# Optimization experiments

Measured on AMD Instinct MI355X. Metric: run time of the kernel, lower is better.

The kernel has to match this reference:

```python
import jax, jax.numpy as jnp
import numpy as np

N_NODES = 100000
N_EDGES = 300000
NUM_GRAPHS = 2000
IN_DIM = 82
HIDDEN = 256


def _gcn_conv(x, src, dst, dinv, W, b):
    # GCNConv: out = D^-1/2 (A + I) D^-1/2 (x W) + b
    xW = x @ W  # [N, H]
    norm = dinv[src] * dinv[dst]  # [E]
    agg = jax.ops.segment_sum(xW[src] * norm[:, None], dst, num_segments=N_NODES)
    self_loop = xW * (dinv * dinv)[:, None]
    return agg + self_loop + b


def setup_inputs() -> dict:
    key = jax.random.key(0)
    ks = jax.random.split(key, 8)
    x = jax.random.normal(ks[0], (N_NODES, IN_DIM), dtype=jnp.float32)
    edge_index = jax.random.randint(ks[1], (2, N_EDGES), 0, N_NODES, dtype=jnp.int64)
    batch = jnp.sort(jax.random.randint(ks[2], (N_NODES,), 0, NUM_GRAPHS, dtype=jnp.int64))
    W1 = jax.random.normal(ks[3], (IN_DIM, HIDDEN), dtype=jnp.float32) * (1.0 / np.sqrt(IN_DIM))
    W2 = jax.random.normal(ks[4], (HIDDEN, HIDDEN), dtype=jnp.float32) * (1.0 / np.sqrt(HIDDEN))
    W3 = jax.random.normal(ks[5], (HIDDEN, HIDDEN), dtype=jnp.float32) * (1.0 / np.sqrt(HIDDEN))
    b1 = jnp.zeros((HIDDEN,), jnp.float32)
    b2 = jnp.zeros((HIDDEN,), jnp.float32)
    b3 = jnp.zeros((HIDDEN,), jnp.float32)
    return {"x": x, "edge_index": edge_index, "batch": batch, "num_graphs": NUM_GRAPHS,
            "W1": W1, "b1": b1, "W2": W2, "b2": b2, "W3": W3, "b3": b3}


def reference(x, edge_index, batch, num_graphs, W1, b1, W2, b2, W3, b3):
    src, dst = edge_index[0], edge_index[1]
    # symmetric normalization with added self-loops (PyG gcn_norm)
    deg = jax.ops.segment_sum(jnp.ones_like(dst, dtype=x.dtype), dst, num_segments=N_NODES) + 1.0
    dinv = jax.lax.rsqrt(deg)
    h = jax.nn.relu(_gcn_conv(x, src, dst, dinv, W1, b1))
    h = jax.nn.relu(_gcn_conv(h, src, dst, dinv, W2, b2))
    h = jax.nn.relu(_gcn_conv(h, src, dst, dinv, W3, b3))
    return jax.ops.segment_max(h, batch, num_segments=num_graphs)  # [G, H]
```

## Files before the change

kernel.cpp:

```cpp
#include <hip/hip_runtime.h>
#include <cstdint>
#include <cstddef>

#define N_NODES 100000
#define N_EDGES 300000
#define N_GRAPHS 2000
#define HID 256
#define INDIM 82
#define K1PAD 128
#define N_TILES ((N_NODES + 255) / 256)
#define SCAN_CHUNK 2048
#define NBLK_SCAN ((N_NODES + SCAN_CHUNK - 1) / SCAN_CHUNK)

typedef __bf16 bf16x8 __attribute__((ext_vector_type(8)));
typedef float f32x4 __attribute__((ext_vector_type(4)));

__device__ __forceinline__ unsigned short f2bf(float f) {
    unsigned int u = __float_as_uint(f);
    u = (u + 0x7fffu + ((u >> 16) & 1u)) >> 16;
    return (unsigned short)u;
}
__device__ __forceinline__ float bf2f(unsigned short s) {
    return __uint_as_float(((unsigned int)s) << 16);
}

__global__ void k_cnt_init(int* cnt) {
    int i = blockIdx.x * 256 + threadIdx.x;
    if (i < N_NODES) cnt[i] = 0;
}

__global__ void k_cnt_acc(const int* __restrict__ ei, int* cnt) {
    int e = blockIdx.x * 256 + threadIdx.x;
    if (e < N_EDGES) atomicAdd(&cnt[ei[N_EDGES + e]], 1);
}

__global__ __launch_bounds__(256) void k_scan1(const int* __restrict__ cnt, int* __restrict__ off,
                                               int* __restrict__ partial) {
    __shared__ int sdata[256];
    const int base = blockIdx.x * SCAN_CHUNK;
    const int t = threadIdx.x;
    int v[8];
    int s = 0;
#pragma unroll
    for (int i = 0; i < 8; ++i) {
        int idx = base + t * 8 + i;
        v[i] = (idx < N_NODES) ? cnt[idx] : 0;
        s += v[i];
    }
    sdata[t] = s;
    __syncthreads();
    for (int d = 1; d < 256; d <<= 1) {
        int x = (t >= d) ? sdata[t - d] : 0;
        __syncthreads();
        sdata[t] += x;
        __syncthreads();
    }
    int run = sdata[t] - s;
#pragma unroll
    for (int i = 0; i < 8; ++i) {
        int idx = base + t * 8 + i;
        if (idx < N_NODES) off[idx] = run;
        run += v[i];
    }
    if (t == 255) partial[blockIdx.x] = sdata[255];
}

__global__ void k_scan2(int* partial) {
    if (threadIdx.x == 0 && blockIdx.x == 0) {
        int run = 0;
        for (int i = 0; i < NBLK_SCAN; ++i) {
            int v = partial[i];
            partial[i] = run;
            run += v;
        }
    }
}

__global__ void k_scan3(int* __restrict__ off, const int* __restrict__ partial,
                        int* __restrict__ cur, const int* __restrict__ cnt,
                        float* __restrict__ dinv) {
    int i = blockIdx.x * 256 + threadIdx.x;
    if (i < N_NODES) {
        int o = off[i] + partial[i >> 11];
        off[i] = o;
        cur[i] = o;
        dinv[i] = rsqrtf((float)cnt[i] + 1.0f);
    }
}

__global__ void k_fill(const int* __restrict__ ei, int* cur, int* __restrict__ csr_src) {
    int e = blockIdx.x * 256 + threadIdx.x;
    if (e < N_EDGES) {
        int s = ei[e];
        int d = ei[N_EDGES + e];
        int pos = atomicAdd(&cur[d], 1);
        csr_src[pos] = s;
    }
}

__global__ void k_bounds(const int* __restrict__ batch, int* __restrict__ gstart) {
    int g = blockIdx.x * 256 + threadIdx.x;
    if (g > N_GRAPHS) return;
    int lo = 0, hi = N_NODES;
    while (lo < hi) {
        int mid = (lo + hi) >> 1;
        if (batch[mid] < g) lo = mid + 1;
        else hi = mid;
    }
    gstart[g] = lo;
}

__global__ void k_xconv(const float* __restrict__ x, unsigned short* __restrict__ xb) {
    int i = blockIdx.x * 256 + threadIdx.x;
    if (i >= N_NODES * K1PAD) return;
    int node = i >> 7;
    int k = i & 127;
    xb[i] = (k < INDIM) ? f2bf(x[(size_t)node * INDIM + k]) : (unsigned short)0;
}

__global__ void k_wconv(const float* __restrict__ W, unsigned short* __restrict__ Wb,
                        int KPAD, int KSRC) {
    int i = blockIdx.x * 256 + threadIdx.x;
    if (i >= 256 * KPAD) return;
    int kc = i >> 13;
    int r = i & 8191;
    int nt = r >> 9;
    int r2 = r & 511;
    int lg = r2 >> 7;
    int lr = (r2 >> 3) & 15;
    int j = r2 & 7;
    int k = kc * 32 + lg * 8 + j;
    int n = nt * 16 + lr;
    Wb[i] = (k < KSRC) ? f2bf(W[(size_t)k * HID + n]) : (unsigned short)0;
}

template <int K>
__global__ __launch_bounds__(512) void k_gemm_mfma(const unsigned short* __restrict__ A,
                                                   const unsigned short* __restrict__ Wb,
                                                   const float* __restrict__ bias,
                                                   unsigned short* __restrict__ Cb) {
    constexpr int NK = K / 32;
    __shared__ __align__(16) unsigned short Wsh[K * HID];

    const int tid = threadIdx.x;
    const int w = tid >> 6;
    const int l = tid & 63;
    const int lr = l & 15;
    const int lg = l >> 4;

#pragma unroll
    for (int i = 0; i < K / 16; ++i) {
        int o = (i * 512 + tid) * 8;
        *reinterpret_cast<uint4*>(&Wsh[o]) = *reinterpret_cast<const uint4*>(Wb + o);
    }
    __syncthreads();

    float bv[16];
#pragma unroll
    for (int nt = 0; nt < 16; ++nt) bv[nt] = bias[nt * 16 + lr];

    for (int t = blockIdx.x; t < N_TILES; t += 256) {
        const int rowbase = t * 256 + w * 32;
        int r0 = rowbase + lr;
        int r1 = rowbase + 16 + lr;
        int r0c = r0 < N_NODES ? r0 : (N_NODES - 1);
        int r1c = r1 < N_NODES ? r1 : (N_NODES - 1);
        const unsigned short* a0p = A + (size_t)r0c * K + lg * 8;
        const unsigned short* a1p = A + (size_t)r1c * K + lg * 8;

        bf16x8 a0[NK], a1[NK];
#pragma unroll
        for (int kc = 0; kc < NK; ++kc) {
            a0[kc] = *reinterpret_cast<const bf16x8*>(a0p + kc * 32);
            a1[kc] = *reinterpret_cast<const bf16x8*>(a1p + kc * 32);
        }

        f32x4 acc0[16] = {};
        f32x4 acc1[16] = {};

#pragma unroll
        for (int kc = 0; kc < NK; ++kc) {
            const unsigned short* bfp = Wsh + kc * 8192 + l * 8;
#pragma unroll
            for (int nt = 0; nt < 16; ++nt) {
                bf16x8 bb = *reinterpret_cast<const bf16x8*>(bfp + nt * 512);
                acc0[nt] = __builtin_amdgcn_mfma_f32_16x16x32_bf16(a0[kc], bb, acc0[nt], 0, 0, 0);
                acc1[nt] = __builtin_amdgcn_mfma_f32_16x16x32_bf16(a1[kc], bb, acc1[nt], 0, 0, 0);
            }
        }

        int gr0 = rowbase + lg * 4;
#pragma unroll
        for (int j = 0; j < 4; ++j) {
            int gr = gr0 + j;
            if (gr < N_NODES) {
                size_t base = (size_t)gr * HID + lr;
#pragma unroll
                for (int nt = 0; nt < 16; ++nt)
                    Cb[base + nt * 16] = f2bf(fmaxf(acc0[nt][j] + bv[nt], 0.0f));
            }
            int gr2 = gr + 16;
            if (gr2 < N_NODES) {
                size_t base = (size_t)gr2 * HID + lr;
#pragma unroll
                for (int nt = 0; nt < 16; ++nt)
                    Cb[base + nt * 16] = f2bf(fmaxf(acc1[nt][j] + bv[nt], 0.0f));
            }
        }
    }
}

__global__ void k_aggregate256(const unsigned short* __restrict__ tb,
                               const float* __restrict__ dinv, const int* __restrict__ off,
                               const int* __restrict__ cnt, const int* __restrict__ csr_src,
                               unsigned short* __restrict__ ob) {
    int node = blockIdx.x * 4 + (threadIdx.x >> 6);
    if (node >= N_NODES) return;
    int lane = threadIdx.x & 63;
    float di = dinv[node];
    float s2 = di * di;
    ushort4 sv = *reinterpret_cast<const ushort4*>(&tb[(size_t)node * HID + lane * 4]);
    float4 acc = {bf2f(sv.x) * s2, bf2f(sv.y) * s2, bf2f(sv.z) * s2, bf2f(sv.w) * s2};

    int o0 = off[node];
    int n = cnt[node];
    int j = 0;
    for (; j + 1 < n; j += 2) {
        int s0 = csr_src[o0 + j];
        int s1 = csr_src[o0 + j + 1];
        float n0 = dinv[s0] * di;
        float n1 = dinv[s1] * di;
        ushort4 u0 = *reinterpret_cast<const ushort4*>(&tb[(size_t)s0 * HID + lane * 4]);
        ushort4 u1 = *reinterpret_cast<const ushort4*>(&tb[(size_t)s1 * HID + lane * 4]);
        acc.x = fmaf(n0, bf2f(u0.x), acc.x);
        acc.y = fmaf(n0, bf2f(u0.y), acc.y);
        acc.z = fmaf(n0, bf2f(u0.z), acc.z);
        acc.w = fmaf(n0, bf2f(u0.w), acc.w);
        acc.x = fmaf(n1, bf2f(u1.x), acc.x);
        acc.y = fmaf(n1, bf2f(u1.y), acc.y);
        acc.z = fmaf(n1, bf2f(u1.z), acc.z);
        acc.w = fmaf(n1, bf2f(u1.w), acc.w);
    }
    if (j < n) {
        int s0 = csr_src[o0 + j];
        float n0 = dinv[s0] * di;
        ushort4 u0 = *reinterpret_cast<const ushort4*>(&tb[(size_t)s0 * HID + lane * 4]);
        acc.x = fmaf(n0, bf2f(u0.x), acc.x);
        acc.y = fmaf(n0, bf2f(u0.y), acc.y);
        acc.z = fmaf(n0, bf2f(u0.z), acc.z);
        acc.w = fmaf(n0, bf2f(u0.w), acc.w);
    }
    ushort4 o;
    o.x = f2bf(acc.x);
    o.y = f2bf(acc.y);
    o.z = f2bf(acc.z);
    o.w = f2bf(acc.w);
    *reinterpret_cast<ushort4*>(&ob[(size_t)node * HID + lane * 4]) = o;
}

__global__ void k_aggregate128(const unsigned short* __restrict__ tb,
                               const float* __restrict__ dinv, const int* __restrict__ off,
                               const int* __restrict__ cnt, const int* __restrict__ csr_src,
                               unsigned short* __restrict__ ob) {
    int node = blockIdx.x * 4 + (threadIdx.x >> 6);
    if (node >= N_NODES) return;
    int lane = threadIdx.x & 63;
    float di = dinv[node];
    float s2 = di * di;
    ushort2 sv = *reinterpret_cast<const ushort2*>(&tb[(size_t)node * K1PAD + lane * 2]);
    float2 acc = {bf2f(sv.x) * s2, bf2f(sv.y) * s2};

    int o0 = off[node];
    int n = cnt[node];
    int j = 0;
    for (; j + 1 < n; j += 2) {
        int s0 = csr_src[o0 + j];
        int s1 = csr_src[o0 + j + 1];
        float n0 = dinv[s0] * di;
        float n1 = dinv[s1] * di;
        ushort2 u0 = *reinterpret_cast<const ushort2*>(&tb[(size_t)s0 * K1PAD + lane * 2]);
        ushort2 u1 = *reinterpret_cast<const ushort2*>(&tb[(size_t)s1 * K1PAD + lane * 2]);
        acc.x = fmaf(n0, bf2f(u0.x), acc.x);
        acc.y = fmaf(n0, bf2f(u0.y), acc.y);
        acc.x = fmaf(n1, bf2f(u1.x), acc.x);
        acc.y = fmaf(n1, bf2f(u1.y), acc.y);
    }
    if (j < n) {
        int s0 = csr_src[o0 + j];
        float n0 = dinv[s0] * di;
        ushort2 u0 = *reinterpret_cast<const ushort2*>(&tb[(size_t)s0 * K1PAD + lane * 2]);
        acc.x = fmaf(n0, bf2f(u0.x), acc.x);
        acc.y = fmaf(n0, bf2f(u0.y), acc.y);
    }
    ushort2 o;
    o.x = f2bf(acc.x);
    o.y = f2bf(acc.y);
    *reinterpret_cast<ushort2*>(&ob[(size_t)node * K1PAD + lane * 2]) = o;
}

__global__ void k_pool2(const unsigned short* __restrict__ hb, const int* __restrict__ gstart,
                        float* __restrict__ out) {
    int g = blockIdx.x;
    int lane = threadIdx.x;
    int s = gstart[g], e = gstart[g + 1];
    float4 m = {0.0f, 0.0f, 0.0f, 0.0f};
    for (int i = s; i < e; ++i) {
        ushort4 u = *reinterpret_cast<const ushort4*>(&hb[(size_t)i * HID + lane * 4]);
        m.x = fmaxf(m.x, bf2f(u.x));
        m.y = fmaxf(m.y, bf2f(u.y));
        m.z = fmaxf(m.z, bf2f(u.z));
        m.w = fmaxf(m.w, bf2f(u.w));
    }
    *reinterpret_cast<float4*>(&out[(size_t)g * HID + lane * 4]) = m;
}

extern "C" void kernel_launch(void* const* d_in, const int* in_sizes, int n_in,
                              void* d_out, int out_size, void* d_ws, size_t ws_size,
                              hipStream_t stream) {
    const float* x = (const float*)d_in[0];
    const int* ei = (const int*)d_in[1];
    const int* batch = (const int*)d_in[2];
    const float* W1 = (const float*)d_in[4];
    const float* b1 = (const float*)d_in[5];
    const float* W2 = (const float*)d_in[6];
    const float* b2 = (const float*)d_in[7];
    const float* W3 = (const float*)d_in[8];
    const float* b3 = (const float*)d_in[9];
    float* out = (float*)d_out;

    char* ws = (char*)d_ws;
    float* dinv = (float*)(ws);
    int* cnt = (int*)(ws + (512 << 10));
    int* off = (int*)(ws + (1024 << 10));
    int* cur = (int*)(ws + (1536 << 10));
    int* part = (int*)(ws + (2048 << 10));
    int* gstart = (int*)(ws + (2048 << 10) + 4096);
    int* csr_src = (int*)(ws + (2176 << 10));
    unsigned short* Wb1 = (unsigned short*)(ws + (3584 << 10));
    unsigned short* Wb2 = (unsigned short*)(ws + (3712 << 10));
    unsigned short* Wb3 = (unsigned short*)(ws + (3904 << 10));
    unsigned short* x_b = (unsigned short*)(ws + (4096 << 10));
    unsigned short* ag1_b = (unsigned short*)(ws + (4096 << 10) + 25600000);
    unsigned short* bufA = (unsigned short*)(ws + (4096 << 10) + 51200000);
    unsigned short* bufB = (unsigned short*)(ws + (4096 << 10) + 102400000);

    const int nblk_nodes = (N_NODES + 255) / 256;
    const int nblk_edges = (N_EDGES + 255) / 256;
    const int nblk_rows4 = (N_NODES + 3) / 4;

    k_cnt_init<<<nblk_nodes, 256, 0, stream>>>(cnt);
    k_cnt_acc<<<nblk_edges, 256, 0, stream>>>(ei, cnt);
    k_scan1<<<NBLK_SCAN, 256, 0, stream>>>(cnt, off, part);
    k_scan2<<<1, 64, 0, stream>>>(part);
    k_scan3<<<nblk_nodes, 256, 0, stream>>>(off, part, cur, cnt, dinv);
    k_fill<<<nblk_edges, 256, 0, stream>>>(ei, cur, csr_src);
    k_bounds<<<(N_GRAPHS + 256) / 256, 256, 0, stream>>>(batch, gstart);

    k_xconv<<<(N_NODES * K1PAD + 255) / 256, 256, 0, stream>>>(x, x_b);
    k_wconv<<<(256 * K1PAD + 255) / 256, 256, 0, stream>>>(W1, Wb1, K1PAD, INDIM);
    k_wconv<<<(256 * HID + 255) / 256, 256, 0, stream>>>(W2, Wb2, HID, HID);
    k_wconv<<<(256 * HID + 255) / 256, 256, 0, stream>>>(W3, Wb3, HID, HID);

    k_aggregate128<<<nblk_rows4, 256, 0, stream>>>(x_b, dinv, off, cnt, csr_src, ag1_b);
    k_gemm_mfma<K1PAD><<<256, 512, 0, stream>>>(ag1_b, Wb1, b1, bufA);

    k_aggregate256<<<nblk_rows4, 256, 0, stream>>>(bufA, dinv, off, cnt, csr_src, bufB);
    k_gemm_mfma<HID><<<256, 512, 0, stream>>>(bufB, Wb2, b2, bufA);

    k_aggregate256<<<nblk_rows4, 256, 0, stream>>>(bufA, dinv, off, cnt, csr_src, bufB);
    k_gemm_mfma<HID><<<256, 512, 0, stream>>>(bufB, Wb3, b3, bufA);

    k_pool2<<<N_GRAPHS, 64, 0, stream>>>(bufA, gstart, out);
}
```

Baseline: 282.7 us.

## Precompute edge norms in CSR, aggregate layer 1 from raw fp32 input, unroll gathers

The CSR fill kernel now stores a per-edge normalization weight, so the aggregation kernels no longer do a dependent dinv[src] gather per edge. The separate fp32-to-bf16 conversion of x is removed: the first-layer aggregation reads the 82-wide fp32 rows directly with 41 active lanes and writes padded bf16. The 256-wide aggregation loop is unrolled by four to keep more gathers in flight, and pooling uses 128 threads per graph. The cost is an extra 1.2 MB norm array and wider fp32 gathers in layer one.

```diff
diff --git a/kernel.cpp b/kernel.cpp
--- a/kernel.cpp
+++ b/kernel.cpp
@@ -88,13 +88,15 @@
     }
 }
 
-__global__ void k_fill(const int* __restrict__ ei, int* cur, int* __restrict__ csr_src) {
+__global__ void k_fill(const int* __restrict__ ei, const float* __restrict__ dinv, int* cur,
+                       int* __restrict__ csr_src, float* __restrict__ csr_norm) {
     int e = blockIdx.x * 256 + threadIdx.x;
     if (e < N_EDGES) {
         int s = ei[e];
         int d = ei[N_EDGES + e];
         int pos = atomicAdd(&cur[d], 1);
         csr_src[pos] = s;
+        csr_norm[pos] = dinv[s] * dinv[d];
     }
 }
 
@@ -108,14 +110,6 @@
         else hi = mid;
     }
     gstart[g] = lo;
-}
-
-__global__ void k_xconv(const float* __restrict__ x, unsigned short* __restrict__ xb) {
-    int i = blockIdx.x * 256 + threadIdx.x;
-    if (i >= N_NODES * K1PAD) return;
-    int node = i >> 7;
-    int k = i & 127;
-    xb[i] = (k < INDIM) ? f2bf(x[(size_t)node * INDIM + k]) : (unsigned short)0;
 }
 
 __global__ void k_wconv(const float* __restrict__ W, unsigned short* __restrict__ Wb,
@@ -213,105 +207,128 @@
 __global__ void k_aggregate256(const unsigned short* __restrict__ tb,
                                const float* __restrict__ dinv, const int* __restrict__ off,
                                const int* __restrict__ cnt, const int* __restrict__ csr_src,
+                               const float* __restrict__ csr_norm,
                                unsigned short* __restrict__ ob) {
     int node = blockIdx.x * 4 + (threadIdx.x >> 6);
     if (node >= N_NODES) return;
     int lane = threadIdx.x & 63;
+    const size_t lo = (size_t)lane * 4;
+    int o0 = off[node];
+    int n = cnt[node];
     float di = dinv[node];
     float s2 = di * di;
-    ushort4 sv = *reinterpret_cast<const ushort4*>(&tb[(size_t)node * HID + lane * 4]);
+    ushort4 sv = *reinterpret_cast<const ushort4*>(&tb[(size_t)node * HID + lo]);
     float4 acc = {bf2f(sv.x) * s2, bf2f(sv.y) * s2, bf2f(sv.z) * s2, bf2f(sv.w) * s2};
 
-    int o0 = off[node];
-    int n = cnt[node];
     int j = 0;
-    for (; j + 1 < n; j += 2) {
+    for (; j + 3 < n; j += 4) {
         int s0 = csr_src[o0 + j];
         int s1 = csr_src[o0 + j + 1];
-        float n0 = dinv[s0] * di;
-        float n1 = dinv[s1] * di;
-        ushort4 u0 = *reinterpret_cast<const ushort4*>(&tb[(size_t)s0 * HID + lane * 4]);
-        ushort4 u1 = *reinterpret_cast<const ushort4*>(&tb[(size_t)s1 * HID + lane * 4]);
-        acc.x = fmaf(n0, bf2f(u0.x), acc.x);
-        acc.y = fmaf(n0, bf2f(u0.y), acc.y);
-        acc.z = fmaf(n0, bf2f(u0.z), acc.z);
-        acc.w = fmaf(n0, bf2f(u0.w), acc.w);
-        acc.x = fmaf(n1, bf2f(u1.x), acc.x);
-        acc.y = fmaf(n1, bf2f(u1.y), acc.y);
-        acc.z = fmaf(n1, bf2f(u1.z), acc.z);
-        acc.w = fmaf(n1, bf2f(u1.w), acc.w);
-    }
-    if (j < n) {
+        int s2i = csr_src[o0 + j + 2];
+        int s3 = csr_src[o0 + j + 3];
+        float n0 = csr_norm[o0 + j];
+        float n1 = csr_norm[o0 + j + 1];
+        float n2 = csr_norm[o0 + j + 2];
+        float n3 = csr_norm[o0 + j + 3];
+        ushort4 u0 = *reinterpret_cast<const ushort4*>(&tb[(size_t)s0 * HID + lo]);
+        ushort4 u1 = *reinterpret_cast<const ushort4*>(&tb[(size_t)s1 * HID + lo]);
+        ushort4 u2 = *reinterpret_cast<const ushort4*>(&tb[(size_t)s2i * HID + lo]);
+        ushort4 u3 = *reinterpret_cast<const ushort4*>(&tb[(size_t)s3 * HID + lo]);
+        acc.x = fmaf(n0, bf2f(u0.x), acc.x); acc.y = fmaf(n0, bf2f(u0.y), acc.y);
+        acc.z = fmaf(n0, bf2f(u0.z), acc.z); acc.w = fmaf(n0, bf2f(u0.w), acc.w);
+        acc.x = fmaf(n1, bf2f(u1.x), acc.x); acc.y = fmaf(n1, bf2f(u1.y), acc.y);
+        acc.z = fmaf(n1, bf2f(u1.z), acc.z); acc.w = fmaf(n1, bf2f(u1.w), acc.w);
+        acc.x = fmaf(n2, bf2f(u2.x), acc.x); acc.y = fmaf(n2, bf2f(u2.y), acc.y);
+        acc.z = fmaf(n2, bf2f(u2.z), acc.z); acc.w = fmaf(n2, bf2f(u2.w), acc.w);
+        acc.x = fmaf(n3, bf2f(u3.x), acc.x); acc.y = fmaf(n3, bf2f(u3.y), acc.y);
+        acc.z = fmaf(n3, bf2f(u3.z), acc.z); acc.w = fmaf(n3, bf2f(u3.w), acc.w);
+    }
+    int rem = n - j;
+    if (rem & 2) {
         int s0 = csr_src[o0 + j];
-        float n0 = dinv[s0] * di;
-        ushort4 u0 = *reinterpret_cast<const ushort4*>(&tb[(size_t)s0 * HID + lane * 4]);
-        acc.x = fmaf(n0, bf2f(u0.x), acc.x);
-        acc.y = fmaf(n0, bf2f(u0.y), acc.y);
-        acc.z = fmaf(n0, bf2f(u0.z), acc.z);
-        acc.w = fmaf(n0, bf2f(u0.w), acc.w);
+        int s1 = csr_src[o0 + j + 1];
+        float n0 = csr_norm[o0 + j];
+        float n1 = csr_norm[o0 + j + 1];
+        ushort4 u0 = *reinterpret_cast<const ushort4*>(&tb[(size_t)s0 * HID + lo]);
+        ushort4 u1 = *reinterpret_cast<const ushort4*>(&tb[(size_t)s1 * HID + lo]);
+        acc.x = fmaf(n0, bf2f(u0.x), acc.x); acc.y = fmaf(n0, bf2f(u0.y), acc.y);
+        acc.z = fmaf(n0, bf2f(u0.z), acc.z); acc.w = fmaf(n0, bf2f(u0.w), acc.w);
+        acc.x = fmaf(n1, bf2f(u1.x), acc.x); acc.y = fmaf(n1, bf2f(u1.y), acc.y);
+        acc.z = fmaf(n1, bf2f(u1.z), acc.z); acc.w = fmaf(n1, bf2f(u1.w), acc.w);
+        j += 2;
+    }
+    if (rem & 1) {
+        int s0 = csr_src[o0 + j];
+        float n0 = csr_norm[o0 + j];
+        ushort4 u0 = *reinterpret_cast<const ushort4*>(&tb[(size_t)s0 * HID + lo]);
+        acc.x = fmaf(n0, bf2f(u0.x), acc.x); acc.y = fmaf(n0, bf2f(u0.y), acc.y);
+        acc.z = fmaf(n0, bf2f(u0.z), acc.z); acc.w = fmaf(n0, bf2f(u0.w), acc.w);
     }
     ushort4 o;
     o.x = f2bf(acc.x);
     o.y = f2bf(acc.y);
     o.z = f2bf(acc.z);
     o.w = f2bf(acc.w);
-    *reinterpret_cast<ushort4*>(&ob[(size_t)node * HID + lane * 4]) = o;
-}
-
-__global__ void k_aggregate128(const unsigned short* __restrict__ tb,
-                               const float* __restrict__ dinv, const int* __restrict__ off,
-                               const int* __restrict__ cnt, const int* __restrict__ csr_src,
-                               unsigned short* __restrict__ ob) {
+    *reinterpret_cast<ushort4*>(&ob[(size_t)node * HID + lo]) = o;
+}
+
+__global__ void k_aggxf(const float* __restrict__ x,
+                        const float* __restrict__ dinv, const int* __restrict__ off,
+                        const int* __restrict__ cnt, const int* __restrict__ csr_src,
+                        const float* __restrict__ csr_norm,
+                        unsigned short* __restrict__ ob) {
     int node = blockIdx.x * 4 + (threadIdx.x >> 6);
     if (node >= N_NODES) return;
     int lane = threadIdx.x & 63;
+    const bool act = lane < 41;
+    const size_t co = (size_t)lane * 2;
+    int o0 = off[node];
+    int n = cnt[node];
     float di = dinv[node];
     float s2 = di * di;
-    ushort2 sv = *reinterpret_cast<const ushort2*>(&tb[(size_t)node * K1PAD + lane * 2]);
-    float2 acc = {bf2f(sv.x) * s2, bf2f(sv.y) * s2};
-
-    int o0 = off[node];
-    int n = cnt[node];
-    int j = 0;
-    for (; j + 1 < n; j += 2) {
-        int s0 = csr_src[o0 + j];
-        int s1 = csr_src[o0 + j + 1];
-        float n0 = dinv[s0] * di;
-        float n1 = dinv[s1] * di;
-        ushort2 u0 = *reinterpret_cast<const ushort2*>(&tb[(size_t)s0 * K1PAD + lane * 2]);
-        ushort2 u1 = *reinterpret_cast<const ushort2*>(&tb[(size_t)s1 * K1PAD + lane * 2]);
-        acc.x = fmaf(n0, bf2f(u0.x), acc.x);
-        acc.y = fmaf(n0, bf2f(u0.y), acc.y);
-        acc.x = fmaf(n1, bf2f(u1.x), acc.x);
-        acc.y = fmaf(n1, bf2f(u1.y), acc.y);
-    }
-    if (j < n) {
-        int s0 = csr_src[o0 + j];
-        float n0 = dinv[s0] * di;
-        ushort2 u0 = *reinterpret_cast<const ushort2*>(&tb[(size_t)s0 * K1PAD + lane * 2]);
-        acc.x = fmaf(n0, bf2f(u0.x), acc.x);
-        acc.y = fmaf(n0, bf2f(u0.y), acc.y);
+    float2 acc = {0.0f, 0.0f};
+    if (act) {
+        float2 sv = *reinterpret_cast<const float2*>(&x[(size_t)node * INDIM + co]);
+        acc.x = sv.x * s2;
+        acc.y = sv.y * s2;
+        int j = 0;
+        for (; j + 1 < n; j += 2) {
+            int s0 = csr_src[o0 + j];
+            int s1 = csr_src[o0 + j + 1];
+            float n0 = csr_norm[o0 + j];
+            float n1 = csr_norm[o0 + j + 1];
+            float2 u0 = *reinterpret_cast<const float2*>(&x[(size_t)s0 * INDIM + co]);
+            float2 u1 = *reinterpret_cast<const float2*>(&x[(size_t)s1 * INDIM + co]);
+            acc.x = fmaf(n0, u0.x, acc.x); acc.y = fmaf(n0, u0.y, acc.y);
+            acc.x = fmaf(n1, u1.x, acc.x); acc.y = fmaf(n1, u1.y, acc.y);
+        }
+        if (j < n) {
+            int s0 = csr_src[o0 + j];
+            float n0 = csr_norm[o0 + j];
+            float2 u0 = *reinterpret_cast<const float2*>(&x[(size_t)s0 * INDIM + co]);
+            acc.x = fmaf(n0, u0.x, acc.x); acc.y = fmaf(n0, u0.y, acc.y);
+        }
     }
     ushort2 o;
     o.x = f2bf(acc.x);
     o.y = f2bf(acc.y);
-    *reinterpret_cast<ushort2*>(&ob[(size_t)node * K1PAD + lane * 2]) = o;
+    *reinterpret_cast<ushort2*>(&ob[(size_t)node * K1PAD + co]) = o;
 }
 
 __global__ void k_pool2(const unsigned short* __restrict__ hb, const int* __restrict__ gstart,
                         float* __restrict__ out) {
     int g = blockIdx.x;
-    int lane = threadIdx.x;
+    int w = threadIdx.x >> 6;
+    int lane = threadIdx.x & 63;
+    int col = w * 128 + lane * 2;
     int s = gstart[g], e = gstart[g + 1];
-    float4 m = {0.0f, 0.0f, 0.0f, 0.0f};
+    float2 m = {0.0f, 0.0f};
     for (int i = s; i < e; ++i) {
-        ushort4 u = *reinterpret_cast<const ushort4*>(&hb[(size_t)i * HID + lane * 4]);
+        ushort2 u = *reinterpret_cast<const ushort2*>(&hb[(size_t)i * HID + col]);
         m.x = fmaxf(m.x, bf2f(u.x));
         m.y = fmaxf(m.y, bf2f(u.y));
-        m.z = fmaxf(m.z, bf2f(u.z));
-        m.w = fmaxf(m.w, bf2f(u.w));
-    }
-    *reinterpret_cast<float4*>(&out[(size_t)g * HID + lane * 4]) = m;
+    }
+    *reinterpret_cast<float2*>(&out[(size_t)g * HID + col]) = m;
 }
 
 extern "C" void kernel_launch(void* const* d_in, const int* in_sizes, int n_in,
@@ -336,13 +353,13 @@
     int* part = (int*)(ws + (2048 << 10));
     int* gstart = (int*)(ws + (2048 << 10) + 4096);
     int* csr_src = (int*)(ws + (2176 << 10));
-    unsigned short* Wb1 = (unsigned short*)(ws + (3584 << 10));
-    unsigned short* Wb2 = (unsigned short*)(ws + (3712 << 10));
-    unsigned short* Wb3 = (unsigned short*)(ws + (3904 << 10));
-    unsigned short* x_b = (unsigned short*)(ws + (4096 << 10));
-    unsigned short* ag1_b = (unsigned short*)(ws + (4096 << 10) + 25600000);
-    unsigned short* bufA = (unsigned short*)(ws + (4096 << 10) + 51200000);
-    unsigned short* bufB = (unsigned short*)(ws + (4096 << 10) + 102400000);
+    float* csr_norm = (float*)(ws + (3392 << 10));
+    unsigned short* Wb1 = (unsigned short*)(ws + (4608 << 10));
+    unsigned short* Wb2 = (unsigned short*)(ws + (4736 << 10));
+    unsigned short* Wb3 = (unsigned short*)(ws + (4928 << 10));
+    unsigned short* ag1_b = (unsigned short*)(ws + (5120 << 10));
+    unsigned short* bufA = (unsigned short*)(ws + (5120 << 10) + 25600000);
+    unsigned short* bufB = (unsigned short*)(ws + (5120 << 10) + 76800000);
 
     const int nblk_nodes = (N_NODES + 255) / 256;
     const int nblk_edges = (N_EDGES + 255) / 256;
@@ -353,22 +370,21 @@
     k_scan1<<<NBLK_SCAN, 256, 0, stream>>>(cnt, off, part);
     k_scan2<<<1, 64, 0, stream>>>(part);
     k_scan3<<<nblk_nodes, 256, 0, stream>>>(off, part, cur, cnt, dinv);
-    k_fill<<<nblk_edges, 256, 0, stream>>>(ei, cur, csr_src);
+    k_fill<<<nblk_edges, 256, 0, stream>>>(ei, dinv, cur, csr_src, csr_norm);
     k_bounds<<<(N_GRAPHS + 256) / 256, 256, 0, stream>>>(batch, gstart);
 
-    k_xconv<<<(N_NODES * K1PAD + 255) / 256, 256, 0, stream>>>(x, x_b);
     k_wconv<<<(256 * K1PAD + 255) / 256, 256, 0, stream>>>(W1, Wb1, K1PAD, INDIM);
     k_wconv<<<(256 * HID + 255) / 256, 256, 0, stream>>>(W2, Wb2, HID, HID);
     k_wconv<<<(256 * HID + 255) / 256, 256, 0, stream>>>(W3, Wb3, HID, HID);
 
-    k_aggregate128<<<nblk_rows4, 256, 0, stream>>>(x_b, dinv, off, cnt, csr_src, ag1_b);
+    k_aggxf<<<nblk_rows4, 256, 0, stream>>>(x, dinv, off, cnt, csr_src, csr_norm, ag1_b);
     k_gemm_mfma<K1PAD><<<256, 512, 0, stream>>>(ag1_b, Wb1, b1, bufA);
 
-    k_aggregate256<<<nblk_rows4, 256, 0, stream>>>(bufA, dinv, off, cnt, csr_src, bufB);
+    k_aggregate256<<<nblk_rows4, 256, 0, stream>>>(bufA, dinv, off, cnt, csr_src, csr_norm, bufB);
     k_gemm_mfma<HID><<<256, 512, 0, stream>>>(bufB, Wb2, b2, bufA);
 
-    k_aggregate256<<<nblk_rows4, 256, 0, stream>>>(bufA, dinv, off, cnt, csr_src, bufB);
+    k_aggregate256<<<nblk_rows4, 256, 0, stream>>>(bufA, dinv, off, cnt, csr_src, csr_norm, bufB);
     k_gemm_mfma<HID><<<256, 512, 0, stream>>>(bufB, Wb3, b3, bufA);
 
-    k_pool2<<<N_GRAPHS, 64, 0, stream>>>(bufA, gstart, out);
-}
+    k_pool2<<<N_GRAPHS, 128, 0, stream>>>(bufA, gstart, out);
+}
```

New measurement: 262.8 us. 7.0% less time.
